# Kernel tuning notes

Measured on AMD Instinct MI355X. Metric: run time of the kernel, lower is better.

## Reference

```python
import jax, jax.numpy as jnp
import numpy as np

D_MODEL = 1024
D = 256
B, T = 64, 512


def setup_inputs() -> dict:
    key = jax.random.key(0)
    ks = jax.random.split(key, 7)
    s = 1.0 / np.sqrt(D_MODEL)
    return {
        "x": jax.random.normal(ks[0], (B, T, D_MODEL), dtype=jnp.float32),
        "Wq": jax.random.uniform(ks[1], (D_MODEL, D), jnp.float32, -s, s),
        "bq": jax.random.uniform(ks[2], (D,), jnp.float32, -s, s),
        "Wk": jax.random.uniform(ks[3], (D_MODEL, D), jnp.float32, -s, s),
        "bk": jax.random.uniform(ks[4], (D,), jnp.float32, -s, s),
        "Wv": jax.random.uniform(ks[5], (D_MODEL, D), jnp.float32, -s, s),
        "bv": jax.random.uniform(ks[6], (D,), jnp.float32, -s, s),
    }


def reference(x, Wq, bq, Wk, bk, Wv, bv):
    # Linear projections: [B,T,d_model] -> [B,T,d]
    q = x @ Wq + bq
    k = x @ Wk + bk
    v = x @ Wv + bv
    Tq = x.shape[1]
    scale = k.shape[-1] ** (-0.5)
    # scores: [B,T,T]
    scores = jnp.einsum('bqd,bkd->bqk', q, k) * scale
    causal = jnp.tril(jnp.ones((Tq, Tq), dtype=bool))
    scores = jnp.where(causal, scores, -jnp.inf)
    weights = jax.nn.softmax(scores, axis=-1)
    out = jnp.einsum('bqk,bkd->bqd', weights, v)
    return out
```

## Files before the change

### kernel.cpp

```cpp
#include <hip/hip_runtime.h>
#include <hip/hip_bf16.h>

typedef __attribute__((ext_vector_type(8))) short short8;
typedef __attribute__((ext_vector_type(4))) float floatx4;

#define GLOAD_LDS16(src, dst) \
  __builtin_amdgcn_global_load_lds((const __attribute__((address_space(1))) unsigned int*)(src), \
      (__attribute__((address_space(3))) unsigned int*)(dst), 16, 0, 0)

__device__ __forceinline__ short f2bf(float f) {
    __hip_bfloat16 h = __float2bfloat16(f);
    return *reinterpret_cast<short*>(&h);
}

__device__ __forceinline__ floatx4 mfma16(short8 a, short8 b, floatx4 c) {
    return __builtin_amdgcn_mfma_f32_16x16x32_bf16(a, b, c, 0, 0, 0);
}

__global__ __launch_bounds__(256) void wconv_kernel(const float* __restrict__ Wq,
                                                    const float* __restrict__ Wk,
                                                    const float* __restrict__ Wv,
                                                    __hip_bfloat16* __restrict__ WT) {
    int n = blockIdx.x;
    const float* W = (n < 256) ? Wq : (n < 512 ? Wk : Wv);
    int nl = n & 255;
    __hip_bfloat16* dst = WT + (size_t)n * 1024;
    for (int kk = threadIdx.x; kk < 1024; kk += 256)
        dst[kk] = __float2bfloat16(W[(size_t)kk * 256 + nl]);
}

__global__ __launch_bounds__(256) void proj_kernel(const float* __restrict__ x,
                                                   const __hip_bfloat16* __restrict__ WT,
                                                   const float* __restrict__ bq,
                                                   const float* __restrict__ bk,
                                                   const float* __restrict__ bv,
                                                   __hip_bfloat16* __restrict__ qo,
                                                   __hip_bfloat16* __restrict__ ko,
                                                   __hip_bfloat16* __restrict__ vo) {
    __shared__ __align__(16) __hip_bfloat16 As[128 * 64];
    __shared__ __align__(16) __hip_bfloat16 Bs[128 * 64];
    char* AsB = (char*)As;
    char* BsB = (char*)Bs;

    const int tid = threadIdx.x;
    const int bid = blockIdx.x;
    const int wgid = (bid & 7) * 192 + (bid >> 3);
    const int ntile = wgid % 6;
    const int m0 = (wgid / 6) * 128;
    const int n0 = ntile * 128;
    const int wid = tid >> 6, lane = tid & 63;
    const int wr = wid >> 1, wc = wid & 1;
    const int l15 = lane & 15, lg = lane >> 4;

    floatx4 acc[4][4];
#pragma unroll
    for (int i = 0; i < 4; ++i)
#pragma unroll
        for (int j = 0; j < 4; ++j) acc[i][j] = (floatx4){0.f, 0.f, 0.f, 0.f};

    const int arow = tid >> 3;
    const int acolb = (tid & 7) * 16;

    for (int kt = 0; kt < 16; ++kt) {
#pragma unroll
        for (int s = 0; s < 4; ++s) {
            int o = s * 4096 + tid * 16;
            int row = o >> 7;
            int so = o ^ ((row & 7) << 4);
            const __hip_bfloat16* src = WT + (size_t)(n0 + row) * 1024 + kt * 64 + ((so & 127) >> 1);
            GLOAD_LDS16(src, BsB + o);
        }
#pragma unroll
        for (int s = 0; s < 4; ++s) {
            int row = s * 32 + arow;
            const float* src = x + (size_t)(m0 + row) * 1024 + kt * 64 + (acolb >> 1);
            floatx4 f0 = *(const floatx4*)src;
            floatx4 f1 = *(const floatx4*)(src + 4);
            short8 h;
            h[0] = f2bf(f0[0]); h[1] = f2bf(f0[1]); h[2] = f2bf(f0[2]); h[3] = f2bf(f0[3]);
            h[4] = f2bf(f1[0]); h[5] = f2bf(f1[1]); h[6] = f2bf(f1[2]); h[7] = f2bf(f1[3]);
            int o = row * 128 + (acolb ^ ((row & 7) << 4));
            *(short8*)(AsB + o) = h;
        }
        __syncthreads();

        short8 af[4][2], bfr[4][2];
#pragma unroll
        for (int mt = 0; mt < 4; ++mt) {
            int row = wr * 64 + mt * 16 + l15;
            int rb = row * 128, msk = (row & 7) << 4;
            af[mt][0] = *(const short8*)(AsB + rb + ((lg * 16) ^ msk));
            af[mt][1] = *(const short8*)(AsB + rb + ((64 + lg * 16) ^ msk));
        }
#pragma unroll
        for (int nt = 0; nt < 4; ++nt) {
            int row = wc * 64 + nt * 16 + l15;
            int rb = row * 128, msk = (row & 7) << 4;
            bfr[nt][0] = *(const short8*)(BsB + rb + ((lg * 16) ^ msk));
            bfr[nt][1] = *(const short8*)(BsB + rb + ((64 + lg * 16) ^ msk));
        }
#pragma unroll
        for (int ks = 0; ks < 2; ++ks)
#pragma unroll
            for (int mt = 0; mt < 4; ++mt)
#pragma unroll
                for (int nt = 0; nt < 4; ++nt)
                    acc[mt][nt] = mfma16(af[mt][ks], bfr[nt][ks], acc[mt][nt]);
        __syncthreads();
    }

    const int mat = ntile >> 1;
    const float* bias = (mat == 0) ? bq : (mat == 1 ? bk : bv);
    __hip_bfloat16* ob = (mat == 0) ? qo : (mat == 1 ? ko : vo);
    const float scale = (mat == 0) ? 0.09016844005556021f : 1.0f;

#pragma unroll
    for (int nt = 0; nt < 4; ++nt) {
        int c = (ntile & 1) * 128 + wc * 64 + nt * 16 + l15;
        float bval = bias[c];
#pragma unroll
        for (int mt = 0; mt < 4; ++mt) {
            int row = m0 + wr * 64 + mt * 16 + lg * 4;
#pragma unroll
            for (int r = 0; r < 4; ++r)
                ob[(size_t)(row + r) * 256 + c] = __float2bfloat16((acc[mt][nt][r] + bval) * scale);
        }
    }
}

__global__ __launch_bounds__(256) void attn_kernel(const __hip_bfloat16* __restrict__ q,
                                                   const __hip_bfloat16* __restrict__ k,
                                                   const __hip_bfloat16* __restrict__ v,
                                                   float* __restrict__ out) {
    __shared__ __align__(16) __hip_bfloat16 Ks[64 * 256];
    __shared__ __align__(16) __hip_bfloat16 VTs[256 * 64];
    __shared__ __align__(16) __hip_bfloat16 Ps[4][16 * 64];
    char* KsB = (char*)Ks;
    char* VTB = (char*)VTs;

    const int tid = threadIdx.x;
    const int bid = blockIdx.x;
    const int wgid = (bid & 7) * 64 + (bid >> 3);
    const int qb = wgid & 7, b = wgid >> 3;
    const int wid = tid >> 6, lane = tid & 63;
    const int l15 = lane & 15, lg = lane >> 4;
    char* PsB = (char*)(&Ps[wid][0]);

    short8 qf[8];
    const __hip_bfloat16* qrow = q + ((size_t)(b * 512 + qb * 64 + wid * 16 + l15)) * 256;
#pragma unroll
    for (int ks = 0; ks < 8; ++ks) qf[ks] = *(const short8*)(qrow + ks * 32 + lg * 8);

    float m_[4], lsum[4];
    floatx4 o[16];
#pragma unroll
    for (int r = 0; r < 4; ++r) { m_[r] = -1e30f; lsum[r] = 0.f; }
#pragma unroll
    for (int dt = 0; dt < 16; ++dt) o[dt] = (floatx4){0.f, 0.f, 0.f, 0.f};

    const int vkv = lane;
    const int vd0 = wid * 8;

    for (int c = 0; c <= qb; ++c) {
        const size_t kvbase = (size_t)(b * 512 + c * 64) * 256;
#pragma unroll
        for (int s = 0; s < 8; ++s) {
            int o_ = s * 4096 + tid * 16;
            int row = o_ >> 9;
            int so = o_ ^ ((row & 7) << 4);
            const __hip_bfloat16* src = k + kvbase + (size_t)row * 256 + ((so & 511) >> 1);
            GLOAD_LDS16(src, KsB + o_);
        }
#pragma unroll
        for (int it = 0; it < 8; ++it) {
            int dbase = vd0 + it * 32;
            short8 vv = *(const short8*)(v + kvbase + (size_t)vkv * 256 + dbase);
#pragma unroll
            for (int j = 0; j < 8; ++j) {
                int d = dbase + j;
                int addr = (d * 128 + vkv * 2) ^ ((d & 7) << 4);
                *(short*)(VTB + addr) = vv[j];
            }
        }
        __syncthreads();

        floatx4 s4[4];
#pragma unroll
        for (int t = 0; t < 4; ++t) s4[t] = (floatx4){0.f, 0.f, 0.f, 0.f};
#pragma unroll
        for (int ks = 0; ks < 8; ++ks) {
#pragma unroll
            for (int t = 0; t < 4; ++t) {
                int kv = t * 16 + l15;
                short8 kf = *(const short8*)(KsB + kv * 512 + ((ks * 64 + lg * 16) ^ ((kv & 7) << 4)));
                s4[t] = mfma16(qf[ks], kf, s4[t]);
            }
        }
        if (c == qb) {
#pragma unroll
            for (int t = 0; t < 4; ++t) {
                int kvl = t * 16 + l15;
#pragma unroll
                for (int r = 0; r < 4; ++r)
                    if (kvl > wid * 16 + lg * 4 + r) s4[t][r] = -1e30f;
            }
        }
        float pm[4], alpha[4], rs[4];
#pragma unroll
        for (int r = 0; r < 4; ++r)
            pm[r] = fmaxf(fmaxf(s4[0][r], s4[1][r]), fmaxf(s4[2][r], s4[3][r]));
#pragma unroll
        for (int off = 1; off <= 8; off <<= 1)
#pragma unroll
            for (int r = 0; r < 4; ++r) pm[r] = fmaxf(pm[r], __shfl_xor(pm[r], off));
#pragma unroll
        for (int r = 0; r < 4; ++r) {
            float mn = fmaxf(m_[r], pm[r]);
            alpha[r] = exp2f(m_[r] - mn);
            m_[r] = mn;
        }
#pragma unroll
        for (int t = 0; t < 4; ++t)
#pragma unroll
            for (int r = 0; r < 4; ++r) s4[t][r] = exp2f(s4[t][r] - m_[r]);
#pragma unroll
        for (int r = 0; r < 4; ++r) rs[r] = s4[0][r] + s4[1][r] + s4[2][r] + s4[3][r];
#pragma unroll
        for (int off = 1; off <= 8; off <<= 1)
#pragma unroll
            for (int r = 0; r < 4; ++r) rs[r] += __shfl_xor(rs[r], off);
#pragma unroll
        for (int r = 0; r < 4; ++r) lsum[r] = lsum[r] * alpha[r] + rs[r];
#pragma unroll
        for (int dt = 0; dt < 16; ++dt) {
            o[dt][0] *= alpha[0]; o[dt][1] *= alpha[1];
            o[dt][2] *= alpha[2]; o[dt][3] *= alpha[3];
        }
#pragma unroll
        for (int t = 0; t < 4; ++t)
#pragma unroll
            for (int r = 0; r < 4; ++r) {
                int qq = lg * 4 + r;
                int addr = (qq * 128 + (t * 16 + l15) * 2) ^ ((qq & 7) << 4);
                *(short*)(PsB + addr) = f2bf(s4[t][r]);
            }
#pragma unroll
        for (int h = 0; h < 2; ++h) {
            short8 pa = *(const short8*)(PsB + l15 * 128 + ((h * 64 + lg * 16) ^ ((l15 & 7) << 4)));
#pragma unroll
            for (int dt = 0; dt < 16; ++dt) {
                int d = dt * 16 + l15;
                short8 vb = *(const short8*)(VTB + d * 128 + ((h * 64 + lg * 16) ^ ((d & 7) << 4)));
                o[dt] = mfma16(pa, vb, o[dt]);
            }
        }
        __syncthreads();
    }

    float inv[4];
#pragma unroll
    for (int r = 0; r < 4; ++r) inv[r] = 1.0f / lsum[r];
    size_t obase = ((size_t)(b * 512 + qb * 64 + wid * 16 + lg * 4)) * 256 + l15;
#pragma unroll
    for (int dt = 0; dt < 16; ++dt)
#pragma unroll
        for (int r = 0; r < 4; ++r)
            out[obase + (size_t)r * 256 + dt * 16] = o[dt][r] * inv[r];
}

extern "C" void kernel_launch(void* const* d_in, const int* in_sizes, int n_in,
                              void* d_out, int out_size, void* d_ws, size_t ws_size,
                              hipStream_t stream) {
    const float* x  = (const float*)d_in[0];
    const float* Wq = (const float*)d_in[1];
    const float* bq = (const float*)d_in[2];
    const float* Wk = (const float*)d_in[3];
    const float* bk = (const float*)d_in[4];
    const float* Wv = (const float*)d_in[5];
    const float* bv = (const float*)d_in[6];
    float* out = (float*)d_out;

    char* ws = (char*)d_ws;
    __hip_bfloat16* WT = (__hip_bfloat16*)ws;
    __hip_bfloat16* qo = (__hip_bfloat16*)(ws + (2u << 20));
    __hip_bfloat16* ko = qo + (size_t)32768 * 256;
    __hip_bfloat16* vo = ko + (size_t)32768 * 256;

    wconv_kernel<<<dim3(768), dim3(256), 0, stream>>>(Wq, Wk, Wv, WT);
    proj_kernel<<<dim3(1536), dim3(256), 0, stream>>>(x, WT, bq, bk, bv, qo, ko, vo);
    attn_kernel<<<dim3(512), dim3(256), 0, stream>>>(qo, ko, vo, out);
}
```

Baseline: 158.1 us.

## Double-buffer weight tiles and load x fragments directly into registers

Reworks the projection GEMM so each wave owns 32 full rows and all 128 columns. The x operand is loaded straight from global memory into registers in MFMA fragment layout and converted to bf16 there, which removes the A tile from LDS. The weight tile is double-buffered in LDS, and the next k-step's global loads (x into registers, W via direct-to-LDS) are issued before the current MFMAs so load latency overlaps compute. The cost is that each wave now re-reads the whole B tile from LDS, and register pressure rises from the prefetched x values.

```diff
diff --git a/kernel.cpp b/kernel.cpp
--- a/kernel.cpp
+++ b/kernel.cpp
@@ -37,9 +37,7 @@
                                                    __hip_bfloat16* __restrict__ qo,
                                                    __hip_bfloat16* __restrict__ ko,
                                                    __hip_bfloat16* __restrict__ vo) {
-    __shared__ __align__(16) __hip_bfloat16 As[128 * 64];
-    __shared__ __align__(16) __hip_bfloat16 Bs[128 * 64];
-    char* AsB = (char*)As;
+    __shared__ __align__(16) __hip_bfloat16 Bs[2][128 * 64];
     char* BsB = (char*)Bs;
 
     const int tid = threadIdx.x;
@@ -49,78 +47,95 @@
     const int m0 = (wgid / 6) * 128;
     const int n0 = ntile * 128;
     const int wid = tid >> 6, lane = tid & 63;
-    const int wr = wid >> 1, wc = wid & 1;
     const int l15 = lane & 15, lg = lane >> 4;
 
-    floatx4 acc[4][4];
-#pragma unroll
-    for (int i = 0; i < 4; ++i)
-#pragma unroll
-        for (int j = 0; j < 4; ++j) acc[i][j] = (floatx4){0.f, 0.f, 0.f, 0.f};
-
-    const int arow = tid >> 3;
-    const int acolb = (tid & 7) * 16;
+    floatx4 acc[2][8];
+#pragma unroll
+    for (int mt = 0; mt < 2; ++mt)
+#pragma unroll
+        for (int nt = 0; nt < 8; ++nt) acc[mt][nt] = (floatx4){0.f, 0.f, 0.f, 0.f};
+
+    const float* xlane = x + (size_t)(m0 + wid * 32 + l15) * 1024 + lg * 8;
+
+    floatx4 ap[2][2][2];
+
+#pragma unroll
+    for (int mt = 0; mt < 2; ++mt)
+#pragma unroll
+        for (int ks = 0; ks < 2; ++ks) {
+            const float* s = xlane + mt * 16 * 1024 + ks * 32;
+            ap[mt][ks][0] = *(const floatx4*)s;
+            ap[mt][ks][1] = *(const floatx4*)(s + 4);
+        }
+#pragma unroll
+    for (int s = 0; s < 4; ++s) {
+        int o = s * 4096 + tid * 16;
+        int row = o >> 7;
+        int so = o ^ ((row & 7) << 4);
+        const __hip_bfloat16* src = WT + (size_t)(n0 + row) * 1024 + ((so & 127) >> 1);
+        GLOAD_LDS16(src, BsB + o);
+    }
+    __syncthreads();
 
     for (int kt = 0; kt < 16; ++kt) {
-#pragma unroll
-        for (int s = 0; s < 4; ++s) {
-            int o = s * 4096 + tid * 16;
-            int row = o >> 7;
-            int so = o ^ ((row & 7) << 4);
-            const __hip_bfloat16* src = WT + (size_t)(n0 + row) * 1024 + kt * 64 + ((so & 127) >> 1);
-            GLOAD_LDS16(src, BsB + o);
-        }
-#pragma unroll
-        for (int s = 0; s < 4; ++s) {
-            int row = s * 32 + arow;
-            const float* src = x + (size_t)(m0 + row) * 1024 + kt * 64 + (acolb >> 1);
-            floatx4 f0 = *(const floatx4*)src;
-            floatx4 f1 = *(const floatx4*)(src + 4);
-            short8 h;
-            h[0] = f2bf(f0[0]); h[1] = f2bf(f0[1]); h[2] = f2bf(f0[2]); h[3] = f2bf(f0[3]);
-            h[4] = f2bf(f1[0]); h[5] = f2bf(f1[1]); h[6] = f2bf(f1[2]); h[7] = f2bf(f1[3]);
-            int o = row * 128 + (acolb ^ ((row & 7) << 4));
-            *(short8*)(AsB + o) = h;
-        }
-        __syncthreads();
-
-        short8 af[4][2], bfr[4][2];
-#pragma unroll
-        for (int mt = 0; mt < 4; ++mt) {
-            int row = wr * 64 + mt * 16 + l15;
-            int rb = row * 128, msk = (row & 7) << 4;
-            af[mt][0] = *(const short8*)(AsB + rb + ((lg * 16) ^ msk));
-            af[mt][1] = *(const short8*)(AsB + rb + ((64 + lg * 16) ^ msk));
-        }
-#pragma unroll
-        for (int nt = 0; nt < 4; ++nt) {
-            int row = wc * 64 + nt * 16 + l15;
-            int rb = row * 128, msk = (row & 7) << 4;
-            bfr[nt][0] = *(const short8*)(BsB + rb + ((lg * 16) ^ msk));
-            bfr[nt][1] = *(const short8*)(BsB + rb + ((64 + lg * 16) ^ msk));
-        }
+        const int buf = kt & 1;
+        short8 afr[2][2];
+#pragma unroll
+        for (int mt = 0; mt < 2; ++mt)
+#pragma unroll
+            for (int ks = 0; ks < 2; ++ks) {
+                short8 h;
+                h[0] = f2bf(ap[mt][ks][0][0]); h[1] = f2bf(ap[mt][ks][0][1]);
+                h[2] = f2bf(ap[mt][ks][0][2]); h[3] = f2bf(ap[mt][ks][0][3]);
+                h[4] = f2bf(ap[mt][ks][1][0]); h[5] = f2bf(ap[mt][ks][1][1]);
+                h[6] = f2bf(ap[mt][ks][1][2]); h[7] = f2bf(ap[mt][ks][1][3]);
+                afr[mt][ks] = h;
+            }
+        if (kt < 15) {
+#pragma unroll
+            for (int mt = 0; mt < 2; ++mt)
+#pragma unroll
+                for (int ks = 0; ks < 2; ++ks) {
+                    const float* s = xlane + mt * 16 * 1024 + (kt + 1) * 64 + ks * 32;
+                    ap[mt][ks][0] = *(const floatx4*)s;
+                    ap[mt][ks][1] = *(const floatx4*)(s + 4);
+                }
+            char* nxt = BsB + (buf ^ 1) * 16384;
+#pragma unroll
+            for (int s = 0; s < 4; ++s) {
+                int o = s * 4096 + tid * 16;
+                int row = o >> 7;
+                int so = o ^ ((row & 7) << 4);
+                const __hip_bfloat16* src = WT + (size_t)(n0 + row) * 1024 + (kt + 1) * 64 + ((so & 127) >> 1);
+                GLOAD_LDS16(src, nxt + o);
+            }
+        }
+        char* cur = BsB + buf * 16384;
 #pragma unroll
         for (int ks = 0; ks < 2; ++ks)
 #pragma unroll
-            for (int mt = 0; mt < 4; ++mt)
-#pragma unroll
-                for (int nt = 0; nt < 4; ++nt)
-                    acc[mt][nt] = mfma16(af[mt][ks], bfr[nt][ks], acc[mt][nt]);
+            for (int nt = 0; nt < 8; ++nt) {
+                int row = nt * 16 + l15;
+                int rb = row * 128, msk = (row & 7) << 4;
+                short8 b8 = *(const short8*)(cur + rb + ((ks * 64 + lg * 16) ^ msk));
+                acc[0][nt] = mfma16(afr[0][ks], b8, acc[0][nt]);
+                acc[1][nt] = mfma16(afr[1][ks], b8, acc[1][nt]);
+            }
         __syncthreads();
     }
 
-    const int mat = ntile >> 1;
-    const float* bias = (mat == 0) ? bq : (mat == 1 ? bk : bv);
-    __hip_bfloat16* ob = (mat == 0) ? qo : (mat == 1 ? ko : vo);
-    const float scale = (mat == 0) ? 0.09016844005556021f : 1.0f;
-
-#pragma unroll
-    for (int nt = 0; nt < 4; ++nt) {
-        int c = (ntile & 1) * 128 + wc * 64 + nt * 16 + l15;
+#pragma unroll
+    for (int nt = 0; nt < 8; ++nt) {
+        int g = n0 + nt * 16 + l15;
+        int mat = g >> 8;
+        const float* bias = (mat == 0) ? bq : (mat == 1 ? bk : bv);
+        __hip_bfloat16* ob = (mat == 0) ? qo : (mat == 1 ? ko : vo);
+        float scale = (mat == 0) ? 0.09016844005556021f : 1.0f;
+        int c = g & 255;
         float bval = bias[c];
 #pragma unroll
-        for (int mt = 0; mt < 4; ++mt) {
-            int row = m0 + wr * 64 + mt * 16 + lg * 4;
+        for (int mt = 0; mt < 2; ++mt) {
+            int row = m0 + wid * 32 + mt * 16 + lg * 4;
 #pragma unroll
             for (int r = 0; r < 4; ++r)
                 ob[(size_t)(row + r) * 256 + c] = __float2bfloat16((acc[mt][nt][r] + bval) * scale);
```

Result: slower. 188.7 us (+19.4%).

## Double-buffer projection GEMM with register prefetch and larger 256-row tiles

Applied to the files above, without the earlier changes.

Rewrites the QKV projection kernel to use 256x128 tiles with 512 threads (8 waves) and double-buffered LDS for A and B. The fp32 x loads are prefetched two k-steps ahead into registers, and the B tiles are staged through async global-to-LDS loads, so memory traffic overlaps the MFMA work. Explicit waitcnt, barriers and setprio control the schedule, and each barrier pair in a k-step replaces two syncthreads. The larger tile halves how often the weights are re-read, at the cost of more LDS and more registers per block.

```diff
diff --git a/kernel.cpp b/kernel.cpp
--- a/kernel.cpp
+++ b/kernel.cpp
@@ -2,6 +2,7 @@
 #include <hip/hip_bf16.h>
 
 typedef __attribute__((ext_vector_type(8))) short short8;
+typedef __attribute__((ext_vector_type(4))) short short4v;
 typedef __attribute__((ext_vector_type(4))) float floatx4;
 
 #define GLOAD_LDS16(src, dst) \
@@ -29,7 +30,7 @@
         dst[kk] = __float2bfloat16(W[(size_t)kk * 256 + nl]);
 }
 
-__global__ __launch_bounds__(256) void proj_kernel(const float* __restrict__ x,
+__global__ __launch_bounds__(512) void proj_kernel(const float* __restrict__ x,
                                                    const __hip_bfloat16* __restrict__ WT,
                                                    const float* __restrict__ bq,
                                                    const float* __restrict__ bk,
@@ -37,90 +38,129 @@
                                                    __hip_bfloat16* __restrict__ qo,
                                                    __hip_bfloat16* __restrict__ ko,
                                                    __hip_bfloat16* __restrict__ vo) {
-    __shared__ __align__(16) __hip_bfloat16 As[128 * 64];
-    __shared__ __align__(16) __hip_bfloat16 Bs[128 * 64];
-    char* AsB = (char*)As;
-    char* BsB = (char*)Bs;
+    __shared__ __align__(16) char Ab[2][32768];
+    __shared__ __align__(16) char Bb[2][16384];
 
     const int tid = threadIdx.x;
     const int bid = blockIdx.x;
-    const int wgid = (bid & 7) * 192 + (bid >> 3);
+    const int wgid = (bid & 7) * 96 + (bid >> 3);
     const int ntile = wgid % 6;
-    const int m0 = (wgid / 6) * 128;
+    const int m0 = (wgid / 6) * 256;
     const int n0 = ntile * 128;
     const int wid = tid >> 6, lane = tid & 63;
-    const int wr = wid >> 1, wc = wid & 1;
+    const int wm = wid >> 1, wn = wid & 1;
     const int l15 = lane & 15, lg = lane >> 4;
 
+    const int ar_row = tid >> 4;
+    const int ar_colf = (tid & 15) * 4;
+    const float* xA = x + (size_t)m0 * 1024;
+
     floatx4 acc[4][4];
 #pragma unroll
     for (int i = 0; i < 4; ++i)
 #pragma unroll
         for (int j = 0; j < 4; ++j) acc[i][j] = (floatx4){0.f, 0.f, 0.f, 0.f};
 
-    const int arow = tid >> 3;
-    const int acolb = (tid & 7) * 16;
-
-    for (int kt = 0; kt < 16; ++kt) {
-#pragma unroll
-        for (int s = 0; s < 4; ++s) {
-            int o = s * 4096 + tid * 16;
-            int row = o >> 7;
-            int so = o ^ ((row & 7) << 4);
-            const __hip_bfloat16* src = WT + (size_t)(n0 + row) * 1024 + kt * 64 + ((so & 127) >> 1);
-            GLOAD_LDS16(src, BsB + o);
-        }
-#pragma unroll
-        for (int s = 0; s < 4; ++s) {
-            int row = s * 32 + arow;
-            const float* src = x + (size_t)(m0 + row) * 1024 + kt * 64 + (acolb >> 1);
-            floatx4 f0 = *(const floatx4*)src;
-            floatx4 f1 = *(const floatx4*)(src + 4);
-            short8 h;
-            h[0] = f2bf(f0[0]); h[1] = f2bf(f0[1]); h[2] = f2bf(f0[2]); h[3] = f2bf(f0[3]);
-            h[4] = f2bf(f1[0]); h[5] = f2bf(f1[1]); h[6] = f2bf(f1[2]); h[7] = f2bf(f1[3]);
-            int o = row * 128 + (acolb ^ ((row & 7) << 4));
-            *(short8*)(AsB + o) = h;
-        }
-        __syncthreads();
-
-        short8 af[4][2], bfr[4][2];
+    floatx4 ra[8], rb[8];
+
+#define STAGE_B(KT, BUFPTR) do {                                                     \
+    _Pragma("unroll")                                                                \
+    for (int s = 0; s < 2; ++s) {                                                    \
+        int o = s * 8192 + tid * 16;                                                 \
+        int row = o >> 7;                                                            \
+        int so = o ^ ((row & 7) << 4);                                               \
+        const __hip_bfloat16* src = WT + (size_t)(n0 + row) * 1024 + (KT) * 64       \
+                                    + ((so & 127) >> 1);                             \
+        GLOAD_LDS16(src, (BUFPTR) + o);                                              \
+    } } while (0)
+
+#define LOAD_A(KT, R) do {                                                           \
+    _Pragma("unroll")                                                                \
+    for (int s = 0; s < 8; ++s)                                                      \
+        R[s] = *(const floatx4*)(xA + (size_t)(s * 32 + ar_row) * 1024               \
+                                 + (KT) * 64 + ar_colf);                             \
+    } while (0)
+
+#define CVT_WRITE_A(R, ABUF) do {                                                    \
+    _Pragma("unroll")                                                                \
+    for (int s = 0; s < 8; ++s) {                                                    \
+        int row = s * 32 + ar_row;                                                   \
+        int addr = row * 128 + ((ar_colf * 2) ^ ((row & 7) << 4));                   \
+        short4v h4;                                                                  \
+        h4[0] = f2bf(R[s][0]); h4[1] = f2bf(R[s][1]);                                \
+        h4[2] = f2bf(R[s][2]); h4[3] = f2bf(R[s][3]);                                \
+        *(short4v*)((ABUF) + addr) = h4;                                             \
+    } } while (0)
+
+#define COMPUTE(ABUF, BBUF) do {                                                     \
+    _Pragma("unroll")                                                                \
+    for (int ks = 0; ks < 2; ++ks) {                                                 \
+        short8 af[4], bf8[4];                                                        \
+        _Pragma("unroll")                                                            \
+        for (int mt = 0; mt < 4; ++mt) {                                             \
+            int row = wm * 64 + mt * 16 + l15;                                       \
+            af[mt] = *(const short8*)((ABUF) + row * 128                             \
+                     + ((ks * 64 + lg * 16) ^ ((row & 7) << 4)));                    \
+        }                                                                            \
+        _Pragma("unroll")                                                            \
+        for (int nt = 0; nt < 4; ++nt) {                                             \
+            int row = wn * 64 + nt * 16 + l15;                                       \
+            bf8[nt] = *(const short8*)((BBUF) + row * 128                            \
+                      + ((ks * 64 + lg * 16) ^ ((row & 7) << 4)));                   \
+        }                                                                            \
+        __builtin_amdgcn_s_setprio(1);                                               \
+        _Pragma("unroll")                                                            \
+        for (int mt = 0; mt < 4; ++mt)                                               \
+            _Pragma("unroll")                                                        \
+            for (int nt = 0; nt < 4; ++nt)                                           \
+                acc[mt][nt] = mfma16(af[mt], bf8[nt], acc[mt][nt]);                  \
+        __builtin_amdgcn_s_setprio(0);                                               \
+    } } while (0)
+
+#define BODY(T, RL, RC) do {                                                         \
+    __builtin_amdgcn_sched_barrier(0);                                               \
+    asm volatile("s_waitcnt vmcnt(10) lgkmcnt(0)" ::: "memory");                     \
+    __builtin_amdgcn_sched_barrier(0);                                               \
+    __builtin_amdgcn_s_barrier();                                                    \
+    __builtin_amdgcn_sched_barrier(0);                                               \
+    { int tp2 = ((T) + 2 > 15) ? 15 : (T) + 2; LOAD_A(tp2, RL); }                    \
+    COMPUTE(Ab[(T) & 1], Bb[(T) & 1]);                                               \
+    __builtin_amdgcn_sched_barrier(0);                                               \
+    __builtin_amdgcn_s_barrier();                                                    \
+    __builtin_amdgcn_sched_barrier(0);                                               \
+    { int tp2 = ((T) + 2 > 15) ? 15 : (T) + 2; STAGE_B(tp2, Bb[(T) & 1]); }          \
+    CVT_WRITE_A(RC, Ab[((T) + 1) & 1]);                                              \
+    } while (0)
+
+    STAGE_B(0, Bb[0]);
+    LOAD_A(0, ra);
+    STAGE_B(1, Bb[1]);
+    LOAD_A(1, rb);
+    CVT_WRITE_A(ra, Ab[0]);
+
+    for (int tt = 0; tt < 8; ++tt) {
+        BODY(2 * tt, ra, rb);
+        BODY(2 * tt + 1, rb, ra);
+    }
+
+#undef BODY
+#undef COMPUTE
+#undef CVT_WRITE_A
+#undef LOAD_A
+#undef STAGE_B
+
+#pragma unroll
+    for (int nt = 0; nt < 4; ++nt) {
+        int g = n0 + wn * 64 + nt * 16 + l15;
+        int mat = g >> 8;
+        const float* bias = (mat == 0) ? bq : (mat == 1 ? bk : bv);
+        __hip_bfloat16* ob = (mat == 0) ? qo : (mat == 1 ? ko : vo);
+        float scale = (mat == 0) ? 0.09016844005556021f : 1.0f;
+        int c = g & 255;
+        float bval = bias[c];
 #pragma unroll
         for (int mt = 0; mt < 4; ++mt) {
-            int row = wr * 64 + mt * 16 + l15;
-            int rb = row * 128, msk = (row & 7) << 4;
-            af[mt][0] = *(const short8*)(AsB + rb + ((lg * 16) ^ msk));
-            af[mt][1] = *(const short8*)(AsB + rb + ((64 + lg * 16) ^ msk));
-        }
-#pragma unroll
-        for (int nt = 0; nt < 4; ++nt) {
-            int row = wc * 64 + nt * 16 + l15;
-            int rb = row * 128, msk = (row & 7) << 4;
-            bfr[nt][0] = *(const short8*)(BsB + rb + ((lg * 16) ^ msk));
-            bfr[nt][1] = *(const short8*)(BsB + rb + ((64 + lg * 16) ^ msk));
-        }
-#pragma unroll
-        for (int ks = 0; ks < 2; ++ks)
-#pragma unroll
-            for (int mt = 0; mt < 4; ++mt)
-#pragma unroll
-                for (int nt = 0; nt < 4; ++nt)
-                    acc[mt][nt] = mfma16(af[mt][ks], bfr[nt][ks], acc[mt][nt]);
-        __syncthreads();
-    }
-
-    const int mat = ntile >> 1;
-    const float* bias = (mat == 0) ? bq : (mat == 1 ? bk : bv);
-    __hip_bfloat16* ob = (mat == 0) ? qo : (mat == 1 ? ko : vo);
-    const float scale = (mat == 0) ? 0.09016844005556021f : 1.0f;
-
-#pragma unroll
-    for (int nt = 0; nt < 4; ++nt) {
-        int c = (ntile & 1) * 128 + wc * 64 + nt * 16 + l15;
-        float bval = bias[c];
-#pragma unroll
-        for (int mt = 0; mt < 4; ++mt) {
-            int row = m0 + wr * 64 + mt * 16 + lg * 4;
+            int row = m0 + wm * 64 + mt * 16 + lg * 4;
 #pragma unroll
             for (int r = 0; r < 4; ++r)
                 ob[(size_t)(row + r) * 256 + c] = __float2bfloat16((acc[mt][nt][r] + bval) * scale);
@@ -287,6 +327,6 @@
     __hip_bfloat16* vo = ko + (size_t)32768 * 256;
 
     wconv_kernel<<<dim3(768), dim3(256), 0, stream>>>(Wq, Wk, Wv, WT);
-    proj_kernel<<<dim3(1536), dim3(256), 0, stream>>>(x, WT, bq, bk, bv, qo, ko, vo);
+    proj_kernel<<<dim3(768), dim3(512), 0, stream>>>(x, WT, bq, bk, bv, qo, ko, vo);
     attn_kernel<<<dim3(512), dim3(256), 0, stream>>>(qo, ko, vo, out);
 }
```

Result: slower. 167.3 us (+5.8%).

## Split projection into Q pass that emits bf16 x, then K/V pass

Applied to the files above, without the earlier changes.

The fused QKV projection re-read fp32 x once for each of its six N tiles. It is replaced by a Q kernel that reads and converts x once, computes Q in a double-buffered pipeline with explicit waitcnt and barriers, and writes a bf16 copy of x to the workspace. A second kernel computes K and V from that bf16 copy, loading it straight into LDS. The aim is less global traffic for x and less repeated conversion work, at the cost of an extra launch and a 64MB bf16 write and read.

```diff
diff --git a/kernel.cpp b/kernel.cpp
--- a/kernel.cpp
+++ b/kernel.cpp
@@ -29,14 +29,141 @@
         dst[kk] = __float2bfloat16(W[(size_t)kk * 256 + nl]);
 }
 
-__global__ __launch_bounds__(256) void proj_kernel(const float* __restrict__ x,
-                                                   const __hip_bfloat16* __restrict__ WT,
-                                                   const float* __restrict__ bq,
-                                                   const float* __restrict__ bk,
-                                                   const float* __restrict__ bv,
-                                                   __hip_bfloat16* __restrict__ qo,
-                                                   __hip_bfloat16* __restrict__ ko,
-                                                   __hip_bfloat16* __restrict__ vo) {
+__global__ __launch_bounds__(512) void projq_kernel(const float* __restrict__ x,
+                                                    const __hip_bfloat16* __restrict__ WT,
+                                                    const float* __restrict__ bq,
+                                                    __hip_bfloat16* __restrict__ qo,
+                                                    __hip_bfloat16* __restrict__ xb) {
+    __shared__ __align__(16) char Ab[2][8192];
+    __shared__ __align__(16) char Bb[2][32768];
+
+    const int tid = threadIdx.x;
+    const int m0 = blockIdx.x * 64;
+    const int wid = tid >> 6, lane = tid & 63;
+    const int wm = wid >> 2, wn = wid & 3;
+    const int l15 = lane & 15, lg = lane >> 4;
+
+    const int arow = tid >> 3;
+    const int acol = (tid & 7) * 8;
+    const float* xr = x + (size_t)(m0 + arow) * 1024 + acol;
+    __hip_bfloat16* xbr = xb + (size_t)(m0 + arow) * 1024 + acol;
+    const int awaddr = arow * 128 + ((acol * 2) ^ ((arow & 7) << 4));
+
+    floatx4 acc[2][4];
+#pragma unroll
+    for (int i = 0; i < 2; ++i)
+#pragma unroll
+        for (int j = 0; j < 4; ++j) acc[i][j] = (floatx4){0.f, 0.f, 0.f, 0.f};
+
+    floatx4 ra[2], rb[2];
+
+#define LOAD_A(KT, R) do {                                                           \
+        R[0] = *(const floatx4*)(xr + (KT) * 64);                                    \
+        R[1] = *(const floatx4*)(xr + (KT) * 64 + 4);                                \
+    } while (0)
+
+#define CVT_STORE(KT, R, ABUF) do {                                                  \
+        short8 h;                                                                    \
+        h[0] = f2bf(R[0][0]); h[1] = f2bf(R[0][1]);                                  \
+        h[2] = f2bf(R[0][2]); h[3] = f2bf(R[0][3]);                                  \
+        h[4] = f2bf(R[1][0]); h[5] = f2bf(R[1][1]);                                  \
+        h[6] = f2bf(R[1][2]); h[7] = f2bf(R[1][3]);                                  \
+        *(short8*)((ABUF) + awaddr) = h;                                             \
+        *(short8*)(xbr + (KT) * 64) = h;                                             \
+    } while (0)
+
+#define STAGE_B(KT, BUF) do {                                                        \
+        _Pragma("unroll")                                                            \
+        for (int s = 0; s < 4; ++s) {                                                \
+            int o = s * 8192 + tid * 16;                                             \
+            int row = o >> 7;                                                        \
+            int so = o ^ ((row & 7) << 4);                                           \
+            const __hip_bfloat16* src = WT + (size_t)row * 1024 + (KT) * 64          \
+                                        + ((so & 127) >> 1);                         \
+            GLOAD_LDS16(src, (BUF) + o);                                             \
+        } } while (0)
+
+#define COMPUTE(ABUF, BBUF) do {                                                     \
+        _Pragma("unroll")                                                            \
+        for (int ks = 0; ks < 2; ++ks) {                                             \
+            short8 af[2], bf8[4];                                                    \
+            _Pragma("unroll")                                                        \
+            for (int mt = 0; mt < 2; ++mt) {                                         \
+                int row = wm * 32 + mt * 16 + l15;                                   \
+                af[mt] = *(const short8*)((ABUF) + row * 128                         \
+                         + ((ks * 64 + lg * 16) ^ ((row & 7) << 4)));                \
+            }                                                                        \
+            _Pragma("unroll")                                                        \
+            for (int nt = 0; nt < 4; ++nt) {                                         \
+                int row = wn * 64 + nt * 16 + l15;                                   \
+                bf8[nt] = *(const short8*)((BBUF) + row * 128                        \
+                          + ((ks * 64 + lg * 16) ^ ((row & 7) << 4)));               \
+            }                                                                        \
+            __builtin_amdgcn_s_setprio(1);                                           \
+            _Pragma("unroll")                                                        \
+            for (int mt = 0; mt < 2; ++mt)                                           \
+                _Pragma("unroll")                                                    \
+                for (int nt = 0; nt < 4; ++nt)                                       \
+                    acc[mt][nt] = mfma16(af[mt], bf8[nt], acc[mt][nt]);              \
+            __builtin_amdgcn_s_setprio(0);                                           \
+        } } while (0)
+
+    LOAD_A(0, ra);
+    STAGE_B(0, Bb[0]);
+    LOAD_A(1, rb);
+    CVT_STORE(0, ra, Ab[0]);
+    __builtin_amdgcn_sched_barrier(0);
+    asm volatile("s_waitcnt vmcnt(3) lgkmcnt(0)" ::: "memory");
+    __builtin_amdgcn_sched_barrier(0);
+    __builtin_amdgcn_s_barrier();
+    __builtin_amdgcn_sched_barrier(0);
+
+#define BODY(T, RL, RC) do {                                                         \
+        int tp1 = ((T) + 1 > 15) ? 15 : (T) + 1;                                     \
+        int tp2 = ((T) + 2 > 15) ? 15 : (T) + 2;                                     \
+        STAGE_B(tp1, Bb[((T) + 1) & 1]);                                             \
+        LOAD_A(tp2, RL);                                                             \
+        COMPUTE(Ab[(T) & 1], Bb[(T) & 1]);                                           \
+        CVT_STORE(tp1, RC, Ab[((T) + 1) & 1]);                                       \
+        __builtin_amdgcn_sched_barrier(0);                                           \
+        asm volatile("s_waitcnt vmcnt(3) lgkmcnt(0)" ::: "memory");                  \
+        __builtin_amdgcn_sched_barrier(0);                                           \
+        __builtin_amdgcn_s_barrier();                                                \
+        __builtin_amdgcn_sched_barrier(0);                                           \
+    } while (0)
+
+    for (int tt = 0; tt < 8; ++tt) {
+        BODY(2 * tt, ra, rb);
+        BODY(2 * tt + 1, rb, ra);
+    }
+
+#undef BODY
+#undef COMPUTE
+#undef STAGE_B
+#undef CVT_STORE
+#undef LOAD_A
+
+    const float scale = 0.09016844005556021f;
+#pragma unroll
+    for (int nt = 0; nt < 4; ++nt) {
+        int c = wn * 64 + nt * 16 + l15;
+        float bval = bq[c];
+#pragma unroll
+        for (int mt = 0; mt < 2; ++mt) {
+            int row = m0 + wm * 32 + mt * 16 + lg * 4;
+#pragma unroll
+            for (int r = 0; r < 4; ++r)
+                qo[(size_t)(row + r) * 256 + c] = __float2bfloat16((acc[mt][nt][r] + bval) * scale);
+        }
+    }
+}
+
+__global__ __launch_bounds__(256) void projkv_kernel(const __hip_bfloat16* __restrict__ xb,
+                                                     const __hip_bfloat16* __restrict__ WT,
+                                                     const float* __restrict__ bk,
+                                                     const float* __restrict__ bv,
+                                                     __hip_bfloat16* __restrict__ ko,
+                                                     __hip_bfloat16* __restrict__ vo) {
     __shared__ __align__(16) __hip_bfloat16 As[128 * 64];
     __shared__ __align__(16) __hip_bfloat16 Bs[128 * 64];
     char* AsB = (char*)As;
@@ -44,10 +171,10 @@
 
     const int tid = threadIdx.x;
     const int bid = blockIdx.x;
-    const int wgid = (bid & 7) * 192 + (bid >> 3);
-    const int ntile = wgid % 6;
-    const int m0 = (wgid / 6) * 128;
-    const int n0 = ntile * 128;
+    const int wgid = (bid & 7) * 128 + (bid >> 3);
+    const int ntile = wgid & 3;
+    const int m0 = (wgid >> 2) * 128;
+    const int n0 = 256 + ntile * 128;
     const int wid = tid >> 6, lane = tid & 63;
     const int wr = wid >> 1, wc = wid & 1;
     const int l15 = lane & 15, lg = lane >> 4;
@@ -57,9 +184,6 @@
     for (int i = 0; i < 4; ++i)
 #pragma unroll
         for (int j = 0; j < 4; ++j) acc[i][j] = (floatx4){0.f, 0.f, 0.f, 0.f};
-
-    const int arow = tid >> 3;
-    const int acolb = (tid & 7) * 16;
 
     for (int kt = 0; kt < 16; ++kt) {
 #pragma unroll
@@ -72,15 +196,11 @@
         }
 #pragma unroll
         for (int s = 0; s < 4; ++s) {
-            int row = s * 32 + arow;
-            const float* src = x + (size_t)(m0 + row) * 1024 + kt * 64 + (acolb >> 1);
-            floatx4 f0 = *(const floatx4*)src;
-            floatx4 f1 = *(const floatx4*)(src + 4);
-            short8 h;
-            h[0] = f2bf(f0[0]); h[1] = f2bf(f0[1]); h[2] = f2bf(f0[2]); h[3] = f2bf(f0[3]);
-            h[4] = f2bf(f1[0]); h[5] = f2bf(f1[1]); h[6] = f2bf(f1[2]); h[7] = f2bf(f1[3]);
-            int o = row * 128 + (acolb ^ ((row & 7) << 4));
-            *(short8*)(AsB + o) = h;
+            int o = s * 4096 + tid * 16;
+            int row = o >> 7;
+            int so = o ^ ((row & 7) << 4);
+            const __hip_bfloat16* src = xb + (size_t)(m0 + row) * 1024 + kt * 64 + ((so & 127) >> 1);
+            GLOAD_LDS16(src, AsB + o);
         }
         __syncthreads();
 
@@ -109,21 +229,20 @@
         __syncthreads();
     }
 
-    const int mat = ntile >> 1;
-    const float* bias = (mat == 0) ? bq : (mat == 1 ? bk : bv);
-    __hip_bfloat16* ob = (mat == 0) ? qo : (mat == 1 ? ko : vo);
-    const float scale = (mat == 0) ? 0.09016844005556021f : 1.0f;
-
 #pragma unroll
     for (int nt = 0; nt < 4; ++nt) {
-        int c = (ntile & 1) * 128 + wc * 64 + nt * 16 + l15;
+        int g = n0 + wc * 64 + nt * 16 + l15;
+        int mat = g >> 8;
+        const float* bias = (mat == 1) ? bk : bv;
+        __hip_bfloat16* ob = (mat == 1) ? ko : vo;
+        int c = g & 255;
         float bval = bias[c];
 #pragma unroll
         for (int mt = 0; mt < 4; ++mt) {
             int row = m0 + wr * 64 + mt * 16 + lg * 4;
 #pragma unroll
             for (int r = 0; r < 4; ++r)
-                ob[(size_t)(row + r) * 256 + c] = __float2bfloat16((acc[mt][nt][r] + bval) * scale);
+                ob[(size_t)(row + r) * 256 + c] = __float2bfloat16(acc[mt][nt][r] + bval);
         }
     }
 }
@@ -285,8 +404,10 @@
     __hip_bfloat16* qo = (__hip_bfloat16*)(ws + (2u << 20));
     __hip_bfloat16* ko = qo + (size_t)32768 * 256;
     __hip_bfloat16* vo = ko + (size_t)32768 * 256;
+    __hip_bfloat16* xb = (__hip_bfloat16*)(ws + 52428800ull);
 
     wconv_kernel<<<dim3(768), dim3(256), 0, stream>>>(Wq, Wk, Wv, WT);
-    proj_kernel<<<dim3(1536), dim3(256), 0, stream>>>(x, WT, bq, bk, bv, qo, ko, vo);
+    projq_kernel<<<dim3(512), dim3(512), 0, stream>>>(x, WT, bq, qo, xb);
+    projkv_kernel<<<dim3(1024), dim3(256), 0, stream>>>(xb, WT, bk, bv, ko, vo);
     attn_kernel<<<dim3(512), dim3(256), 0, stream>>>(qo, ko, vo, out);
 }
```

Result: slower. 177.4 us (+12.2%).
